# Kernel tuning notes

Measured on AMD Instinct MI355X. Metric: run time of the kernel, lower is better.

The kernel has to match this reference:

```python
import jax, jax.numpy as jnp
import numpy as np

N_NODES = 10000
N_EDGES = 320000
F_NODE = 16
NUM_BESSEL = 8
M = 32           # env_embed_multiplicity
LAT = 128        # latent dimension
R_MAX = 5.0
P_CUT = 6.0      # polynomial cutoff order
AVG_NEIGH = 32.0
SQRT3 = 1.7320508075688772
SQRT2 = 1.4142135623730951


def _mlp(x, weights):
    # nequip ScalarMLPFunction: linear layers with 1/sqrt(fan_in) norm, silu between layers
    h = x
    n = len(weights)
    for i, W in enumerate(weights):
        h = h @ W * (1.0 / np.sqrt(W.shape[0]))
        if i < n - 1:
            h = jax.nn.silu(h)
    return h


def _weight_channels(Y, w):
    # MakeWeightedChannels: Y [E,4] = (0e | 1e), w [E,M,2] per-irrep weights -> [E,M,4]
    return jnp.concatenate([w[..., 0:1] * Y[:, None, 0:1],
                            w[..., 1:2] * Y[:, None, 1:4]], axis=-1)


def setup_inputs():
    key = jax.random.key(0)
    ks = jax.random.split(key, 16)

    def w(k, i, o):
        return jax.random.normal(k, (i, o), jnp.float32)

    two_body_in = 2 * F_NODE + NUM_BESSEL  # 40
    return {
        "coordinates": jax.random.uniform(ks[0], (N_NODES, 3), jnp.float32),
        "node_attrs": jax.random.uniform(ks[1], (N_NODES, F_NODE), jnp.float32),
        "edge_index": jax.random.randint(ks[2], (2, N_EDGES), 0, N_NODES),
        "W2b0": w(ks[3], two_body_in, 64),
        "W2b1": w(ks[4], 64, 128),
        "W2b2": w(ks[5], 128, LAT),
        "Wenv0": w(ks[6], LAT, 4 * M),       # initial-edge embed + env weights (2 irreps each)
        "Wlat0": w(ks[7], LAT + 2 * M, 128),
        "Wlat1": w(ks[8], 128, LAT),
        "Ws0": w(ks[9], 2 * M, M),            # e3nn Linear, scalar block (2 paths)
        "Wv0": w(ks[10], 3 * M, M),           # e3nn Linear, vector block (3 paths)
        "Wenv1": w(ks[11], LAT, 2 * M),
        "Wfin0": w(ks[12], LAT + 2 * M, 128),
        "Wfin1": w(ks[13], 128, LAT),
    }


def reference(coordinates, node_attrs, edge_index, W2b0, W2b1, W2b2, Wenv0,
              Wlat0, Wlat1, Ws0, Wv0, Wenv1, Wfin0, Wfin1):
    sender, center = edge_index[0], edge_index[1]
    vec = coordinates[center] - coordinates[sender]            # [E,3]
    r = jnp.sqrt(jnp.sum(vec * vec, axis=-1) + 1e-12)          # [E]
    u = r / R_MAX
    p = P_CUT
    fcut = (1.0 - (p + 1.0) * (p + 2.0) / 2.0 * u**p
            + p * (p + 2.0) * u**(p + 1.0)
            - p * (p + 1.0) / 2.0 * u**(p + 2.0))
    fcut = jnp.where(u < 1.0, fcut, 0.0)
    n = jnp.arange(1, NUM_BESSEL + 1, dtype=jnp.float32)
    bessel = np.sqrt(2.0 / R_MAX) * jnp.sin(n * jnp.pi * u[:, None]) / r[:, None]
    edge_feats = bessel * fcut[:, None]                        # [E,8]
    unit = vec / r[:, None]
    Y = jnp.concatenate([jnp.ones_like(r)[:, None], SQRT3 * unit], axis=-1)  # [E,4] component-normalized SH

    inv_sqrt_n = 1.0 / np.sqrt(AVG_NEIGH)
    E = r.shape[0]

    # two-body latent (layer 0)
    lat_in = jnp.concatenate([node_attrs[center], node_attrs[sender], edge_feats], -1)
    lat = _mlp(lat_in, (W2b0, W2b1, W2b2)) * fcut[:, None]     # [E,LAT]
    w_all = lat @ Wenv0 * (1.0 / np.sqrt(LAT))                 # [E,4M]
    w_edge = w_all[:, :2 * M].reshape(E, M, 2)
    w_env = w_all[:, 2 * M:].reshape(E, M, 2)
    feat = _weight_channels(Y, w_edge)                         # [E,M,4] initial edge embed
    env = jax.ops.segment_sum(_weight_channels(Y, w_env), center, num_segments=N_NODES)
    env = env[center] * inv_sqrt_n                             # [E,M,4]

    fs, fv = feat[..., 0], feat[..., 1:]
    es, ev = env[..., 0], env[..., 1:]
    # layer-0 tensor product instruction list (uuu, no weights)
    p0 = fs * es                               # 0e x 0e -> 0e
    p1 = jnp.sum(fv * ev, -1) / SQRT3          # 1e x 1e -> 0e
    p2 = fs[..., None] * ev                    # 0e x 1e -> 1e
    p3 = fv * es[..., None]                    # 1e x 0e -> 1e
    p4 = jnp.cross(fv, ev) / SQRT2             # 1e x 1e -> 1e
    scal0 = jnp.concatenate([p0, p1], -1)      # [E,2M] scalar outs (n_scalar_outs=2)
    # per-layer e3nn Linear
    s_mix = scal0 @ Ws0 * (1.0 / np.sqrt(2 * M))                         # [E,M]
    v_mix = jnp.einsum('eic,io->eoc', jnp.concatenate([p2, p3, p4], 1), Wv0) * (1.0 / np.sqrt(3 * M))  # [E,M,3]

    # latent resnet update (update param 0 -> sigmoid = 0.5)
    alpha = 0.5
    c_old = 1.0 / np.sqrt(alpha * alpha + 1.0)
    c_new = alpha * c_old
    new_lat = _mlp(jnp.concatenate([lat, scal0], -1), (Wlat0, Wlat1)) * fcut[:, None]
    lat = c_old * lat + c_new * new_lat

    # layer 1 env embedding + tensor product (last layer -> scalars only)
    w_env1 = (lat @ Wenv1 * (1.0 / np.sqrt(LAT))).reshape(E, M, 2)
    env1 = jax.ops.segment_sum(_weight_channels(Y, w_env1), center, num_segments=N_NODES)
    env1 = env1[center] * inv_sqrt_n
    q0 = s_mix * env1[..., 0]
    q1 = jnp.sum(v_mix * env1[..., 1:], -1) / SQRT3
    scal1 = jnp.concatenate([q0, q1], -1)      # [E,2M]

    new_lat = _mlp(jnp.concatenate([lat, scal1], -1), (Wfin0, Wfin1)) * fcut[:, None]
    lat = c_old * lat + c_new * new_lat

    node_out = jax.ops.segment_sum(lat, center, num_segments=N_NODES) * inv_sqrt_n
    return node_out
```

## Files before the change

kernel.cpp:

```cpp
#include <hip/hip_runtime.h>
#include <hip/hip_bf16.h>
#include <math.h>

typedef __hip_bfloat16 bf16;
typedef __attribute__((ext_vector_type(8))) short short8;
typedef __attribute__((ext_vector_type(4))) float floatx4;

#define AMODE_PLAIN  0
#define AMODE_CONCAT 2
#define EPI_SPLIT    1
#define EPI_STORE    2
#define EPI_FCUT     3
#define EPI_RESID    4

#define INV_SQRT_N 0.17677669529663687f
#define INV_SQRT3  0.5773502691896258f
#define INV_SQRT2  0.7071067811865476f
#define C_OLD      0.8944271909999159f
#define C_NEW      0.4472135954999579f
#define PI_F       3.14159265358979323846f
#define SQRT3_F    1.7320508075688772f
#define BESSEL_PREF 0.6324555320336759f

__device__ __forceinline__ float b2f(bf16 x) { return __bfloat162float(x); }
__device__ __forceinline__ bf16  f2b(float x) { return __float2bfloat16(x); }
__device__ __forceinline__ unsigned short f2bu(float x) {
  bf16 h = f2b(x); unsigned short u; __builtin_memcpy(&u, &h, 2); return u;
}
__device__ __forceinline__ float silu_f(float v) { return v / (1.f + __expf(-v)); }
__device__ __forceinline__ floatx4 mfma16(short8 a, short8 b, floatx4 c) {
  return __builtin_amdgcn_mfma_f32_16x16x32_bf16(a, b, c, 0, 0, 0);
}

__global__ __launch_bounds__(256) void k_geom(
    const float* __restrict__ coords, const float* __restrict__ nattr,
    const int* __restrict__ eidx, int E,
    float* __restrict__ fcut, float* __restrict__ Yb, bf16* __restrict__ a40) {
  int e = blockIdx.x * 256 + threadIdx.x;
  if (e >= E) return;
  int s = eidx[e], c = eidx[E + e];
  float dx = coords[c*3+0] - coords[s*3+0];
  float dy = coords[c*3+1] - coords[s*3+1];
  float dz = coords[c*3+2] - coords[s*3+2];
  float r = sqrtf(dx*dx + dy*dy + dz*dz + 1e-12f);
  float u = r * 0.2f;
  float u3 = u*u*u;
  float u6 = u3*u3, u7 = u6*u, u8 = u7*u;
  float fc = 1.f - 28.f*u6 + 48.f*u7 - 21.f*u8;
  fc = (u < 1.f) ? fc : 0.f;
  float inv_r = 1.f / r;
  fcut[e] = fc;
  Yb[e*4+0] = 1.f;
  Yb[e*4+1] = SQRT3_F * dx * inv_r;
  Yb[e*4+2] = SQRT3_F * dy * inv_r;
  Yb[e*4+3] = SQRT3_F * dz * inv_r;
  bf16* row = a40 + (long)e * 40;
  #pragma unroll
  for (int i = 0; i < 16; ++i) row[i]      = f2b(nattr[(long)c*16 + i]);
  #pragma unroll
  for (int i = 0; i < 16; ++i) row[16 + i] = f2b(nattr[(long)s*16 + i]);
  float pref = BESSEL_PREF * inv_r * fc;
  #pragma unroll
  for (int n = 1; n <= 8; ++n)
    row[32 + n - 1] = f2b(pref * sinf((float)n * PI_F * u));
}

__global__ __launch_bounds__(256) void k_deg(
    const int* __restrict__ eidx, int E, int* __restrict__ deg) {
  int e = blockIdx.x * 256 + threadIdx.x;
  if (e < E) atomicAdd(&deg[eidx[E + e]], 1);
}

__global__ __launch_bounds__(1024) void k_scan(
    const int* __restrict__ deg, int N,
    int* __restrict__ rowptr, int* __restrict__ cursor) {
  __shared__ int part[1024];
  int t = threadIdx.x;
  int C = (N + 1023) / 1024;
  int base = t * C;
  int s = 0;
  for (int i = 0; i < C; ++i) { int idx = base + i; if (idx < N) s += deg[idx]; }
  part[t] = s;
  __syncthreads();
  for (int off = 1; off < 1024; off <<= 1) {
    int v = (t >= off) ? part[t - off] : 0;
    __syncthreads();
    part[t] += v;
    __syncthreads();
  }
  int excl = (t == 0) ? 0 : part[t - 1];
  for (int i = 0; i < C; ++i) {
    int idx = base + i;
    if (idx < N) { rowptr[idx] = excl; cursor[idx] = excl; excl += deg[idx]; }
  }
  if (t == 0) rowptr[N] = part[1023];
}

__global__ __launch_bounds__(256) void k_fill(
    const int* __restrict__ eidx, int E, int* __restrict__ cursor,
    int* __restrict__ eord) {
  int e = blockIdx.x * 256 + threadIdx.x;
  if (e >= E) return;
  int c = eidx[E + e];
  int slot = atomicAdd(&cursor[c], 1);
  eord[slot] = e;
}

__global__ __launch_bounds__(256) void k_wprep(
    const float* __restrict__ W, unsigned short* __restrict__ Wt, int K, int NOUT) {
  int t = blockIdx.x * 256 + threadIdx.x;
  if (t >= K * NOUT) return;
  int n = t / K, k = t % K;
  Wt[n * K + k] = f2bu(W[k * NOUT + n]);
}

__global__ __launch_bounds__(256) void k_wmix(
    const float* __restrict__ Ws0, const float* __restrict__ Wv0,
    unsigned short* __restrict__ Wm) {
  int t = blockIdx.x * 256 + threadIdx.x;
  if (t >= 32 * 160) return;
  int o = t / 160, k = t % 160;
  float v = (k < 64) ? Ws0[k * 32 + o] : Wv0[(k - 64) * 32 + o];
  Wm[o * 160 + k] = f2bu(v);
}

__global__ __launch_bounds__(256) void k_envg(
    const bf16* __restrict__ wenv, const float* __restrict__ Yb,
    const int* __restrict__ rowptr, const int* __restrict__ eord,
    int N, float* __restrict__ env) {
  int t = blockIdx.x * 256 + threadIdx.x;
  if (t >= N * 32) return;
  int n = t >> 5, m = t & 31;
  int j0 = rowptr[n], j1 = rowptr[n + 1];
  float a0 = 0.f, a1 = 0.f, a2 = 0.f, a3 = 0.f;
  for (int j = j0; j < j1; ++j) {
    int e = eord[j];
    float w0 = b2f(wenv[(long)e*64 + 2*m]);
    float w1 = b2f(wenv[(long)e*64 + 2*m + 1]);
    float4 y = *reinterpret_cast<const float4*>(&Yb[(long)e*4]);
    a0 += w0;
    a1 += w1 * y.y;
    a2 += w1 * y.z;
    a3 += w1 * y.w;
  }
  *reinterpret_cast<float4*>(&env[(long)n*128 + m*4]) = make_float4(a0, a1, a2, a3);
}

__global__ __launch_bounds__(256) void k_nodeg(
    const bf16* __restrict__ lat, const int* __restrict__ rowptr,
    const int* __restrict__ eord, int N, float* __restrict__ out) {
  int t = blockIdx.x * 256 + threadIdx.x;
  if (t >= N * 128) return;
  int n = t >> 7, j = t & 127;
  int j0 = rowptr[n], j1 = rowptr[n + 1];
  float s = 0.f;
  for (int q = j0; q < j1; ++q) {
    int e = eord[q];
    s += b2f(lat[(long)e*128 + j]);
  }
  out[t] = s * INV_SQRT_N;
}

__global__ __launch_bounds__(256) void mgemm40(
    const bf16* __restrict__ A, const unsigned short* __restrict__ Wt,
    bf16* __restrict__ out, float scale, int E) {
  __shared__ __align__(16) unsigned short As[64 * 72];
  __shared__ __align__(16) unsigned short Bs[64 * 72];
  int tid = threadIdx.x;
  int lane = tid & 63, w = tid >> 6;
  int nl = lane & 15, quad = lane >> 4;
  long e0 = (long)blockIdx.x * 64;

  for (int i = tid; i < 512; i += 256) {
    int e = i >> 3, h = i & 7;
    short8 v = {0,0,0,0,0,0,0,0};
    long eg = e0 + e;
    if (h < 5 && eg < E) v = *(const short8*)(A + eg * 40 + h * 8);
    *(short8*)&As[e * 72 + h * 8] = v;
  }
  for (int i = tid; i < 512; i += 256) {
    int n = i >> 3, h = i & 7;
    short8 v = {0,0,0,0,0,0,0,0};
    if (h < 5) v = *(const short8*)(Wt + n * 40 + h * 8);
    *(short8*)&Bs[n * 72 + h * 8] = v;
  }
  __syncthreads();

  floatx4 acc[4];
  #pragma unroll
  for (int i = 0; i < 4; ++i) acc[i] = (floatx4){0.f,0.f,0.f,0.f};
  #pragma unroll
  for (int ks = 0; ks < 2; ++ks) {
    short8 af[4];
    #pragma unroll
    for (int et = 0; et < 4; ++et)
      af[et] = *(const short8*)&As[(et*16 + nl) * 72 + ks*32 + quad*8];
    short8 bv = *(const short8*)&Bs[(w*16 + nl) * 72 + ks*32 + quad*8];
    #pragma unroll
    for (int et = 0; et < 4; ++et) acc[et] = mfma16(af[et], bv, acc[et]);
  }
  #pragma unroll
  for (int et = 0; et < 4; ++et)
    #pragma unroll
    for (int r = 0; r < 4; ++r) {
      long eg = e0 + et*16 + quad*4 + r;
      if (eg >= E) continue;
      out[eg * 64 + w*16 + nl] = f2b(silu_f(acc[et][r] * scale));
    }
}

template<int K, int NOUT, int EPI>
__global__ __launch_bounds__(256) void mgemm(
    const bf16* __restrict__ A, const unsigned short* __restrict__ Wt,
    bf16* __restrict__ out1, bf16* __restrict__ out2, float scale, int E) {
  constexpr int KP = 40;
  constexpr int CT = NOUT / 64;
  __shared__ __align__(16) unsigned short As[64 * KP];
  __shared__ __align__(16) unsigned short Bs[NOUT * KP];
  int tid = threadIdx.x;
  int lane = tid & 63, w = tid >> 6;
  int nl = lane & 15, quad = lane >> 4;
  long e0 = (long)blockIdx.x * 64;

  floatx4 acc[4][CT];
  #pragma unroll
  for (int i = 0; i < 4; ++i)
    #pragma unroll
    for (int j = 0; j < CT; ++j) acc[i][j] = (floatx4){0.f,0.f,0.f,0.f};

  int ae = tid & 63, akh = tid >> 6;
  long aeg = e0 + ae;

  for (int k0 = 0; k0 < K; k0 += 32) {
    if (k0) __syncthreads();
    {
      short8 v = {0,0,0,0,0,0,0,0};
      if (aeg < E) v = *(const short8*)(A + aeg * (long)K + k0 + akh * 8);
      *(short8*)&As[ae * KP + akh * 8] = v;
    }
    if constexpr (NOUT == 128) {
      int j = tid >> 1, h = tid & 1;
      const short8* s = (const short8*)(Wt + (long)j * K + k0 + h * 16);
      *(short8*)&Bs[j * KP + h * 16]     = s[0];
      *(short8*)&Bs[j * KP + h * 16 + 8] = s[1];
    } else {
      int j = tid >> 2, h = tid & 3;
      *(short8*)&Bs[j * KP + h * 8] =
          *(const short8*)(Wt + (long)j * K + k0 + h * 8);
    }
    __syncthreads();
    short8 af[4], bv[CT];
    #pragma unroll
    for (int et = 0; et < 4; ++et)
      af[et] = *(const short8*)&As[(et*16 + nl) * KP + quad * 8];
    #pragma unroll
    for (int ct = 0; ct < CT; ++ct)
      bv[ct] = *(const short8*)&Bs[(w*CT*16 + ct*16 + nl) * KP + quad * 8];
    #pragma unroll
    for (int et = 0; et < 4; ++et)
      #pragma unroll
      for (int ct = 0; ct < CT; ++ct)
        acc[et][ct] = mfma16(af[et], bv[ct], acc[et][ct]);
  }

  #pragma unroll
  for (int et = 0; et < 4; ++et)
    #pragma unroll
    for (int ct = 0; ct < CT; ++ct)
      #pragma unroll
      for (int r = 0; r < 4; ++r) {
        long eg = e0 + et*16 + quad*4 + r;
        if (eg >= E) continue;
        int col = w*CT*16 + ct*16 + nl;
        float v = acc[et][ct][r] * scale;
        if constexpr (EPI == EPI_SPLIT) {
          if (col < 64) out1[eg * 64 + col] = f2b(v);
          else          out2[eg * 64 + (col - 64)] = f2b(v);
        } else {
          out1[eg * NOUT + col] = f2b(v);
        }
      }
}

template<int K, int AMODE, int EPI>
__global__ __launch_bounds__(256) void mfused(
    const bf16* __restrict__ A, const bf16* __restrict__ A2,
    const unsigned short* __restrict__ W0t, const unsigned short* __restrict__ W1t,
    bf16* __restrict__ outb, const float* __restrict__ fcut,
    float scale0, float scale1, int E) {
  constexpr int KP = 40, HP = 136;
  __shared__ __align__(16) unsigned short As[64 * KP];
  __shared__ __align__(16) unsigned short Bs[128 * KP];
  __shared__ __align__(16) unsigned short Hs[64 * HP];
  int tid = threadIdx.x;
  int lane = tid & 63, w = tid >> 6;
  int nl = lane & 15, quad = lane >> 4;
  long e0 = (long)blockIdx.x * 64;

  floatx4 acc[4][2];
  #pragma unroll
  for (int i = 0; i < 4; ++i)
    #pragma unroll
    for (int j = 0; j < 2; ++j) acc[i][j] = (floatx4){0.f,0.f,0.f,0.f};

  int ae = tid & 63, akh = tid >> 6;
  long aeg = e0 + ae;
  int bj = tid >> 1, bh = tid & 1;

  for (int k0 = 0; k0 < K; k0 += 32) {
    if (k0) __syncthreads();
    {
      int kk = k0 + akh * 8;
      short8 v = {0,0,0,0,0,0,0,0};
      if (aeg < E) {
        const bf16* src;
        if constexpr (AMODE == AMODE_PLAIN) src = A + aeg * (long)K + kk;
        else src = (kk < 128) ? (A + aeg * 128 + kk) : (A2 + aeg * 64 + (kk - 128));
        v = *(const short8*)src;
      }
      *(short8*)&As[ae * KP + akh * 8] = v;
    }
    {
      const short8* s = (const short8*)(W0t + (long)bj * K + k0 + bh * 16);
      *(short8*)&Bs[bj * KP + bh * 16]     = s[0];
      *(short8*)&Bs[bj * KP + bh * 16 + 8] = s[1];
    }
    __syncthreads();
    short8 af[4], bv[2];
    #pragma unroll
    for (int et = 0; et < 4; ++et)
      af[et] = *(const short8*)&As[(et*16 + nl) * KP + quad * 8];
    #pragma unroll
    for (int ct = 0; ct < 2; ++ct)
      bv[ct] = *(const short8*)&Bs[(w*32 + ct*16 + nl) * KP + quad * 8];
    #pragma unroll
    for (int et = 0; et < 4; ++et)
      #pragma unroll
      for (int ct = 0; ct < 2; ++ct)
        acc[et][ct] = mfma16(af[et], bv[ct], acc[et][ct]);
  }

  #pragma unroll
  for (int et = 0; et < 4; ++et)
    #pragma unroll
    for (int ct = 0; ct < 2; ++ct)
      #pragma unroll
      for (int r = 0; r < 4; ++r) {
        int el = et*16 + quad*4 + r;
        int h  = w*32 + ct*16 + nl;
        Hs[el * HP + h] = f2bu(silu_f(acc[et][ct][r] * scale0));
      }
  #pragma unroll
  for (int i = 0; i < 4; ++i)
    #pragma unroll
    for (int j = 0; j < 2; ++j) acc[i][j] = (floatx4){0.f,0.f,0.f,0.f};

  for (int k0 = 0; k0 < 128; k0 += 32) {
    __syncthreads();
    {
      const short8* s = (const short8*)(W1t + (long)bj * 128 + k0 + bh * 16);
      *(short8*)&Bs[bj * KP + bh * 16]     = s[0];
      *(short8*)&Bs[bj * KP + bh * 16 + 8] = s[1];
    }
    __syncthreads();
    short8 af[4], bv[2];
    #pragma unroll
    for (int et = 0; et < 4; ++et)
      af[et] = *(const short8*)&Hs[(et*16 + nl) * HP + k0 + quad * 8];
    #pragma unroll
    for (int ct = 0; ct < 2; ++ct)
      bv[ct] = *(const short8*)&Bs[(w*32 + ct*16 + nl) * KP + quad * 8];
    #pragma unroll
    for (int et = 0; et < 4; ++et)
      #pragma unroll
      for (int ct = 0; ct < 2; ++ct)
        acc[et][ct] = mfma16(af[et], bv[ct], acc[et][ct]);
  }

  #pragma unroll
  for (int et = 0; et < 4; ++et)
    #pragma unroll
    for (int ct = 0; ct < 2; ++ct)
      #pragma unroll
      for (int r = 0; r < 4; ++r) {
        long eg = e0 + et*16 + quad*4 + r;
        if (eg >= E) continue;
        int col = w*32 + ct*16 + nl;
        float fc = fcut[eg];
        float v = acc[et][ct][r] * scale1 * fc;
        if constexpr (EPI == EPI_FCUT) {
          outb[eg * 128 + col] = f2b(v);
        } else {
          long idx = eg * 128 + col;
          outb[idx] = f2b(C_OLD * b2f(outb[idx]) + C_NEW * v);
        }
      }
}

__global__ __launch_bounds__(256) void k_prod(
    const bf16* __restrict__ wedge, const float* __restrict__ env,
    const float* __restrict__ Yb, const int* __restrict__ eidx, int E,
    bf16* __restrict__ scal) {
  long t = (long)blockIdx.x * 256 + threadIdx.x;
  if (t >= (long)E * 32) return;
  long e = t >> 5;
  int m = (int)(t & 31);
  int c = eidx[E + e];
  float w0 = b2f(wedge[e*64 + 2*m]), w1 = b2f(wedge[e*64 + 2*m + 1]);
  const float* ep = env + (long)c*128 + m*4;
  float es  = ep[0] * INV_SQRT_N;
  float evx = ep[1] * INV_SQRT_N, evy = ep[2] * INV_SQRT_N, evz = ep[3] * INV_SQRT_N;
  float y1 = Yb[e*4+1], y2 = Yb[e*4+2], y3 = Yb[e*4+3];
  float fvx = w1*y1, fvy = w1*y2, fvz = w1*y3;
  scal[e*64 + m]      = f2b(w0 * es);
  scal[e*64 + 32 + m] = f2b((fvx*evx + fvy*evy + fvz*evz) * INV_SQRT3);
}

__global__ __launch_bounds__(256) void k_mix2(
    const bf16* __restrict__ wedge, const float* __restrict__ env,
    const float* __restrict__ env1, const float* __restrict__ Yb,
    const int* __restrict__ eidx, const unsigned short* __restrict__ Wm,
    int E, bf16* __restrict__ scal) {
  constexpr int PP = 360;
  constexpr int RP = 132;
  __shared__ __align__(16) unsigned char SB[64 * PP * 2];
  __shared__ __align__(16) unsigned short Wl[32 * 160];
  unsigned short* P = (unsigned short*)SB;
  float* R = (float*)SB;
  int tid = threadIdx.x;
  int lane = tid & 63, w = tid >> 6;
  int nl = lane & 15, quad = lane >> 4;
  long e0 = (long)blockIdx.x * 64;

  for (int i = tid; i < 640; i += 256)
    *(short8*)&Wl[i * 8] = *(const short8*)(Wm + i * 8);

  int m = tid & 31;
  #pragma unroll
  for (int it = 0; it < 8; ++it) {
    int el = (tid >> 5) + it * 8;
    long e = e0 + el;
    if (e < E) {
      int c = eidx[E + e];
      float w0 = b2f(wedge[e*64 + 2*m]), w1 = b2f(wedge[e*64 + 2*m + 1]);
      float4 ev4 = *(const float4*)(env + (long)c*128 + m*4);
      float4 y   = *(const float4*)(Yb + e*4);
      float es  = ev4.x * INV_SQRT_N;
      float evx = ev4.y * INV_SQRT_N, evy = ev4.z * INV_SQRT_N, evz = ev4.w * INV_SQRT_N;
      float fvx = w1*y.y, fvy = w1*y.z, fvz = w1*y.w;
      unsigned short* p = P + el * PP;
      p[m]       = f2bu(w0 * es);
      p[32 + m]  = f2bu((fvx*evx + fvy*evy + fvz*evz) * INV_SQRT3);
      p[64 + m]  = f2bu(w0 * evx);
      p[96 + m]  = f2bu(fvx * es);
      p[128 + m] = f2bu((fvy*evz - fvz*evy) * INV_SQRT2);
      p[160 + m] = f2bu(w0 * evy);
      p[192 + m] = f2bu(fvy * es);
      p[224 + m] = f2bu((fvz*evx - fvx*evz) * INV_SQRT2);
      p[256 + m] = f2bu(w0 * evz);
      p[288 + m] = f2bu(fvz * es);
      p[320 + m] = f2bu((fvx*evy - fvy*evx) * INV_SQRT2);
    } else {
      unsigned short* p = P + el * PP;
      #pragma unroll
      for (int q = 0; q < 11; ++q) p[q*32 + m] = 0;
    }
  }
  __syncthreads();

  floatx4 acc[4][2];
  #pragma unroll
  for (int i = 0; i < 4; ++i)
    #pragma unroll
    for (int j = 0; j < 2; ++j) acc[i][j] = (floatx4){0.f,0.f,0.f,0.f};
  int pbase  = (w == 0) ? 0 : 64 + (w - 1) * 96;
  int wkbase = (w == 0) ? 0 : 64;
  int ksteps = (w == 0) ? 2 : 3;
  for (int ks = 0; ks < ksteps; ++ks) {
    short8 af[4], bv[2];
    #pragma unroll
    for (int et = 0; et < 4; ++et)
      af[et] = *(const short8*)&P[(et*16 + nl) * PP + pbase + ks*32 + quad*8];
    #pragma unroll
    for (int ct = 0; ct < 2; ++ct)
      bv[ct] = *(const short8*)&Wl[(ct*16 + nl) * 160 + wkbase + ks*32 + quad*8];
    #pragma unroll
    for (int et = 0; et < 4; ++et)
      #pragma unroll
      for (int ct = 0; ct < 2; ++ct)
        acc[et][ct] = mfma16(af[et], bv[ct], acc[et][ct]);
  }
  __syncthreads();

  #pragma unroll
  for (int et = 0; et < 4; ++et)
    #pragma unroll
    for (int ct = 0; ct < 2; ++ct)
      #pragma unroll
      for (int r = 0; r < 4; ++r) {
        int el = et*16 + quad*4 + r;
        R[el * RP + w*32 + ct*16 + nl] = acc[et][ct][r];
      }
  __syncthreads();

  #pragma unroll
  for (int it = 0; it < 8; ++it) {
    int el = (tid >> 5) + it * 8;
    long e = e0 + el;
    if (e >= E) continue;
    int o = m;
    int c = eidx[E + e];
    float4 e1 = *(const float4*)(env1 + (long)c*128 + o*4);
    float sr = R[el * RP + o];
    float vx = R[el * RP + 32 + o];
    float vy = R[el * RP + 64 + o];
    float vz = R[el * RP + 96 + o];
    float q0 = sr * 0.125f * (e1.x * INV_SQRT_N);
    float q1 = (vx*e1.y + vy*e1.z + vz*e1.w) *
               (0.10206207261596577f * INV_SQRT_N * INV_SQRT3);
    scal[e*64 + o]      = f2b(q0);
    scal[e*64 + 32 + o] = f2b(q1);
  }
}

extern "C" void kernel_launch(void* const* d_in, const int* in_sizes, int n_in,
                              void* d_out, int out_size, void* d_ws, size_t ws_size,
                              hipStream_t stream) {
  const float* coords = (const float*)d_in[0];
  const float* nattr  = (const float*)d_in[1];
  const int*   eidx   = (const int*)d_in[2];
  const float* W2b0   = (const float*)d_in[3];
  const float* W2b1   = (const float*)d_in[4];
  const float* W2b2   = (const float*)d_in[5];
  const float* Wenv0  = (const float*)d_in[6];
  const float* Wlat0  = (const float*)d_in[7];
  const float* Wlat1  = (const float*)d_in[8];
  const float* Ws0    = (const float*)d_in[9];
  const float* Wv0    = (const float*)d_in[10];
  const float* Wenv1  = (const float*)d_in[11];
  const float* Wfin0  = (const float*)d_in[12];
  const float* Wfin1  = (const float*)d_in[13];
  float* out = (float*)d_out;
  int E = in_sizes[2] / 2;
  int N = in_sizes[0] / 3;

  float* fcut   = (float*)d_ws;
  float* Yb     = fcut + (size_t)E;
  float* env    = Yb + (size_t)E*4;
  float* env1   = env + (size_t)N*128;
  int*   deg    = (int*)(env1 + (size_t)N*128);
  int*   rowptr = deg + N;
  int*   cursor = rowptr + (N + 8);
  int*   eord   = cursor + N;
  bf16*  b64    = (bf16*)(eord + E);
  bf16*  lat    = b64 + (size_t)E*64;
  bf16*  S      = lat + (size_t)E*128;
  unsigned short* W2b1t  = (unsigned short*)(S + (size_t)E*64);
  unsigned short* W2b2t  = W2b1t + 128*64;
  unsigned short* Wenv0t = W2b2t + 128*128;
  unsigned short* Wlat0t = Wenv0t + 128*128;
  unsigned short* Wlat1t = Wlat0t + 128*192;
  unsigned short* Wenv1t = Wlat1t + 128*128;
  unsigned short* Wfin0t = Wenv1t + 64*128;
  unsigned short* Wfin1t = Wfin0t + 128*192;
  unsigned short* W2b0t  = Wfin1t + 128*128;
  unsigned short* Wmixt  = W2b0t + 64*40;

  hipMemsetAsync(deg, 0, (size_t)N * sizeof(int), stream);

  dim3 blk(256);
  const float s40  = 0.15811388300841897f;
  const float s64  = 0.125f;
  const float s128 = 0.08838834764831845f;
  const float s192 = 0.07216878364870323f;
  int gB = (E + 63) / 64;
  int gE = (E + 255) / 256;

  k_geom<<<gE, blk, 0, stream>>>(coords, nattr, eidx, E, fcut, Yb, S );
  k_deg<<<gE, blk, 0, stream>>>(eidx, E, deg);
  k_scan<<<1, 1024, 0, stream>>>(deg, N, rowptr, cursor);
  k_fill<<<gE, blk, 0, stream>>>(eidx, E, cursor, eord);
  k_wprep<<<(64*128 + 255)/256,  blk, 0, stream>>>(W2b1,  W2b1t,  64, 128);
  k_wprep<<<(128*128 + 255)/256, blk, 0, stream>>>(W2b2,  W2b2t,  128, 128);
  k_wprep<<<(128*128 + 255)/256, blk, 0, stream>>>(Wenv0, Wenv0t, 128, 128);
  k_wprep<<<(192*128 + 255)/256, blk, 0, stream>>>(Wlat0, Wlat0t, 192, 128);
  k_wprep<<<(128*128 + 255)/256, blk, 0, stream>>>(Wlat1, Wlat1t, 128, 128);
  k_wprep<<<(128*64 + 255)/256,  blk, 0, stream>>>(Wenv1, Wenv1t, 128, 64);
  k_wprep<<<(192*128 + 255)/256, blk, 0, stream>>>(Wfin0, Wfin0t, 192, 128);
  k_wprep<<<(128*128 + 255)/256, blk, 0, stream>>>(Wfin1, Wfin1t, 128, 128);
  k_wprep<<<(40*64 + 255)/256,   blk, 0, stream>>>(W2b0,  W2b0t,  40, 64);
  k_wmix<<<(32*160 + 255)/256,   blk, 0, stream>>>(Ws0, Wv0, Wmixt);

  mgemm40<<<gB, blk, 0, stream>>>(S , W2b0t, b64, s40, E);
  mfused<64,AMODE_PLAIN,EPI_FCUT><<<gB, blk, 0, stream>>>(
      b64, nullptr, W2b1t, W2b2t, lat, fcut, s64, s128, E);

  mgemm<128,128,EPI_SPLIT><<<gB, blk, 0, stream>>>(
      lat, Wenv0t, b64, S , s128, E);

  k_envg<<<dim3((N*32 + 255) / 256), blk, 0, stream>>>(
      S , Yb, rowptr, eord, N, env);

  k_prod<<<dim3((int)(((long)E*32 + 255) / 256)), blk, 0, stream>>>(
      b64, env, Yb, eidx, E, S );

  mfused<192,AMODE_CONCAT,EPI_RESID><<<gB, blk, 0, stream>>>(
      lat, S , Wlat0t, Wlat1t, lat, fcut, s192, s128, E);

  mgemm<128,64,EPI_STORE><<<gB, blk, 0, stream>>>(
      lat, Wenv1t, S , nullptr, s128, E);

  k_envg<<<dim3((N*32 + 255) / 256), blk, 0, stream>>>(
      S , Yb, rowptr, eord, N, env1);

  k_mix2<<<gB, blk, 0, stream>>>(
      b64, env, env1, Yb, eidx, Wmixt, E, S );

  mfused<192,AMODE_CONCAT,EPI_RESID><<<gB, blk, 0, stream>>>(
      lat, S , Wfin0t, Wfin1t, lat, fcut, s192, s128, E);

  k_nodeg<<<dim3((N*128 + 255) / 256), blk, 0, stream>>>(
      lat, rowptr, eord, N, out);
}
```

Before: 829.1 us.

## Process edges in center-sorted order and merge weight prep kernels

The geometry kernel now writes every per-edge buffer in CSR (center-sorted) order, so all later edge kernels work on sorted edges. The gather-style segment reductions (env and node output) can then read contiguous rows instead of going through the eord indirection. A cent array replaces the eidx center lookups, which also gives the env gathers better locality. The ten weight-transpose launches are folded into one kernel to cut launch overhead. The sorted order is set by the atomic fill order, so it is not deterministic from run to run.

New measurement: 724.1 us. 12.7% less time.

```diff
diff --git a/kernel.cpp b/kernel.cpp
--- a/kernel.cpp
+++ b/kernel.cpp
@@ -30,39 +30,6 @@
 __device__ __forceinline__ float silu_f(float v) { return v / (1.f + __expf(-v)); }
 __device__ __forceinline__ floatx4 mfma16(short8 a, short8 b, floatx4 c) {
   return __builtin_amdgcn_mfma_f32_16x16x32_bf16(a, b, c, 0, 0, 0);
-}
-
-__global__ __launch_bounds__(256) void k_geom(
-    const float* __restrict__ coords, const float* __restrict__ nattr,
-    const int* __restrict__ eidx, int E,
-    float* __restrict__ fcut, float* __restrict__ Yb, bf16* __restrict__ a40) {
-  int e = blockIdx.x * 256 + threadIdx.x;
-  if (e >= E) return;
-  int s = eidx[e], c = eidx[E + e];
-  float dx = coords[c*3+0] - coords[s*3+0];
-  float dy = coords[c*3+1] - coords[s*3+1];
-  float dz = coords[c*3+2] - coords[s*3+2];
-  float r = sqrtf(dx*dx + dy*dy + dz*dz + 1e-12f);
-  float u = r * 0.2f;
-  float u3 = u*u*u;
-  float u6 = u3*u3, u7 = u6*u, u8 = u7*u;
-  float fc = 1.f - 28.f*u6 + 48.f*u7 - 21.f*u8;
-  fc = (u < 1.f) ? fc : 0.f;
-  float inv_r = 1.f / r;
-  fcut[e] = fc;
-  Yb[e*4+0] = 1.f;
-  Yb[e*4+1] = SQRT3_F * dx * inv_r;
-  Yb[e*4+2] = SQRT3_F * dy * inv_r;
-  Yb[e*4+3] = SQRT3_F * dz * inv_r;
-  bf16* row = a40 + (long)e * 40;
-  #pragma unroll
-  for (int i = 0; i < 16; ++i) row[i]      = f2b(nattr[(long)c*16 + i]);
-  #pragma unroll
-  for (int i = 0; i < 16; ++i) row[16 + i] = f2b(nattr[(long)s*16 + i]);
-  float pref = BESSEL_PREF * inv_r * fc;
-  #pragma unroll
-  for (int n = 1; n <= 8; ++n)
-    row[32 + n - 1] = f2b(pref * sinf((float)n * PI_F * u));
 }
 
 __global__ __launch_bounds__(256) void k_deg(
@@ -98,46 +65,93 @@
 
 __global__ __launch_bounds__(256) void k_fill(
     const int* __restrict__ eidx, int E, int* __restrict__ cursor,
-    int* __restrict__ eord) {
+    int* __restrict__ eord, int* __restrict__ cent) {
   int e = blockIdx.x * 256 + threadIdx.x;
   if (e >= E) return;
   int c = eidx[E + e];
   int slot = atomicAdd(&cursor[c], 1);
   eord[slot] = e;
-}
-
-__global__ __launch_bounds__(256) void k_wprep(
-    const float* __restrict__ W, unsigned short* __restrict__ Wt, int K, int NOUT) {
-  int t = blockIdx.x * 256 + threadIdx.x;
-  if (t >= K * NOUT) return;
+  cent[slot] = c;
+}
+
+__global__ __launch_bounds__(256) void k_geom(
+    const float* __restrict__ coords, const float* __restrict__ nattr,
+    const int* __restrict__ eidx, const int* __restrict__ eord, int E,
+    float* __restrict__ fcut, float* __restrict__ Yb, bf16* __restrict__ a40) {
+  int j = blockIdx.x * 256 + threadIdx.x;
+  if (j >= E) return;
+  int e = eord[j];
+  int s = eidx[e], c = eidx[E + e];
+  float dx = coords[c*3+0] - coords[s*3+0];
+  float dy = coords[c*3+1] - coords[s*3+1];
+  float dz = coords[c*3+2] - coords[s*3+2];
+  float r = sqrtf(dx*dx + dy*dy + dz*dz + 1e-12f);
+  float u = r * 0.2f;
+  float u3 = u*u*u;
+  float u6 = u3*u3, u7 = u6*u, u8 = u7*u;
+  float fc = 1.f - 28.f*u6 + 48.f*u7 - 21.f*u8;
+  fc = (u < 1.f) ? fc : 0.f;
+  float inv_r = 1.f / r;
+  fcut[j] = fc;
+  Yb[j*4+0] = 1.f;
+  Yb[j*4+1] = SQRT3_F * dx * inv_r;
+  Yb[j*4+2] = SQRT3_F * dy * inv_r;
+  Yb[j*4+3] = SQRT3_F * dz * inv_r;
+  bf16* row = a40 + (long)j * 40;
+  #pragma unroll
+  for (int i = 0; i < 16; ++i) row[i]      = f2b(nattr[(long)c*16 + i]);
+  #pragma unroll
+  for (int i = 0; i < 16; ++i) row[16 + i] = f2b(nattr[(long)s*16 + i]);
+  float pref = BESSEL_PREF * inv_r * fc;
+  #pragma unroll
+  for (int n = 1; n <= 8; ++n)
+    row[32 + n - 1] = f2b(pref * sinf((float)n * PI_F * u));
+}
+
+__device__ __forceinline__ void wp(const float* W, unsigned short* Wt,
+                                   int K, int NOUT, int t) {
   int n = t / K, k = t % K;
   Wt[n * K + k] = f2bu(W[k * NOUT + n]);
 }
 
-__global__ __launch_bounds__(256) void k_wmix(
-    const float* __restrict__ Ws0, const float* __restrict__ Wv0,
-    unsigned short* __restrict__ Wm) {
+__global__ __launch_bounds__(256) void k_wprep_all(
+    const float* W2b0, const float* W2b1, const float* W2b2,
+    const float* Wenv0, const float* Wlat0, const float* Wlat1,
+    const float* Wenv1, const float* Wfin0, const float* Wfin1,
+    const float* Ws0, const float* Wv0,
+    unsigned short* W2b0t, unsigned short* W2b1t, unsigned short* W2b2t,
+    unsigned short* Wenv0t, unsigned short* Wlat0t, unsigned short* Wlat1t,
+    unsigned short* Wenv1t, unsigned short* Wfin0t, unsigned short* Wfin1t,
+    unsigned short* Wmixt) {
   int t = blockIdx.x * 256 + threadIdx.x;
-  if (t >= 32 * 160) return;
-  int o = t / 160, k = t % 160;
-  float v = (k < 64) ? Ws0[k * 32 + o] : Wv0[(k - 64) * 32 + o];
-  Wm[o * 160 + k] = f2bu(v);
+  if (t < 8192)  { wp(W2b1,  W2b1t,  64, 128, t); return; } t -= 8192;
+  if (t < 16384) { wp(W2b2,  W2b2t, 128, 128, t); return; } t -= 16384;
+  if (t < 16384) { wp(Wenv0, Wenv0t,128, 128, t); return; } t -= 16384;
+  if (t < 24576) { wp(Wlat0, Wlat0t,192, 128, t); return; } t -= 24576;
+  if (t < 16384) { wp(Wlat1, Wlat1t,128, 128, t); return; } t -= 16384;
+  if (t < 8192)  { wp(Wenv1, Wenv1t,128,  64, t); return; } t -= 8192;
+  if (t < 24576) { wp(Wfin0, Wfin0t,192, 128, t); return; } t -= 24576;
+  if (t < 16384) { wp(Wfin1, Wfin1t,128, 128, t); return; } t -= 16384;
+  if (t < 2560)  { wp(W2b0,  W2b0t,  40,  64, t); return; } t -= 2560;
+  if (t < 5120) {
+    int o = t / 160, k = t % 160;
+    float v = (k < 64) ? Ws0[k * 32 + o] : Wv0[(k - 64) * 32 + o];
+    Wmixt[o * 160 + k] = f2bu(v);
+  }
 }
 
 __global__ __launch_bounds__(256) void k_envg(
     const bf16* __restrict__ wenv, const float* __restrict__ Yb,
-    const int* __restrict__ rowptr, const int* __restrict__ eord,
-    int N, float* __restrict__ env) {
+    const int* __restrict__ rowptr, int N, float* __restrict__ env) {
   int t = blockIdx.x * 256 + threadIdx.x;
   if (t >= N * 32) return;
   int n = t >> 5, m = t & 31;
   int j0 = rowptr[n], j1 = rowptr[n + 1];
   float a0 = 0.f, a1 = 0.f, a2 = 0.f, a3 = 0.f;
   for (int j = j0; j < j1; ++j) {
-    int e = eord[j];
-    float w0 = b2f(wenv[(long)e*64 + 2*m]);
-    float w1 = b2f(wenv[(long)e*64 + 2*m + 1]);
-    float4 y = *reinterpret_cast<const float4*>(&Yb[(long)e*4]);
+    float w0 = b2f(wenv[(long)j*64 + 2*m]);
+    float w1 = b2f(wenv[(long)j*64 + 2*m + 1]);
+    float4 y = *reinterpret_cast<const float4*>(&Yb[(long)j*4]);
     a0 += w0;
     a1 += w1 * y.y;
     a2 += w1 * y.z;
@@ -148,16 +162,14 @@
 
 __global__ __launch_bounds__(256) void k_nodeg(
     const bf16* __restrict__ lat, const int* __restrict__ rowptr,
-    const int* __restrict__ eord, int N, float* __restrict__ out) {
+    int N, float* __restrict__ out) {
   int t = blockIdx.x * 256 + threadIdx.x;
   if (t >= N * 128) return;
   int n = t >> 7, j = t & 127;
   int j0 = rowptr[n], j1 = rowptr[n + 1];
   float s = 0.f;
-  for (int q = j0; q < j1; ++q) {
-    int e = eord[q];
-    s += b2f(lat[(long)e*128 + j]);
-  }
+  for (int q = j0; q < j1; ++q)
+    s += b2f(lat[(long)q*128 + j]);
   out[t] = s * INV_SQRT_N;
 }
 
@@ -399,13 +411,13 @@
 
 __global__ __launch_bounds__(256) void k_prod(
     const bf16* __restrict__ wedge, const float* __restrict__ env,
-    const float* __restrict__ Yb, const int* __restrict__ eidx, int E,
+    const float* __restrict__ Yb, const int* __restrict__ cent, int E,
     bf16* __restrict__ scal) {
   long t = (long)blockIdx.x * 256 + threadIdx.x;
   if (t >= (long)E * 32) return;
   long e = t >> 5;
   int m = (int)(t & 31);
-  int c = eidx[E + e];
+  int c = cent[e];
   float w0 = b2f(wedge[e*64 + 2*m]), w1 = b2f(wedge[e*64 + 2*m + 1]);
   const float* ep = env + (long)c*128 + m*4;
   float es  = ep[0] * INV_SQRT_N;
@@ -419,7 +431,7 @@
 __global__ __launch_bounds__(256) void k_mix2(
     const bf16* __restrict__ wedge, const float* __restrict__ env,
     const float* __restrict__ env1, const float* __restrict__ Yb,
-    const int* __restrict__ eidx, const unsigned short* __restrict__ Wm,
+    const int* __restrict__ cent, const unsigned short* __restrict__ Wm,
     int E, bf16* __restrict__ scal) {
   constexpr int PP = 360;
   constexpr int RP = 132;
@@ -441,7 +453,7 @@
     int el = (tid >> 5) + it * 8;
     long e = e0 + el;
     if (e < E) {
-      int c = eidx[E + e];
+      int c = cent[e];
       float w0 = b2f(wedge[e*64 + 2*m]), w1 = b2f(wedge[e*64 + 2*m + 1]);
       float4 ev4 = *(const float4*)(env + (long)c*128 + m*4);
       float4 y   = *(const float4*)(Yb + e*4);
@@ -509,7 +521,7 @@
     long e = e0 + el;
     if (e >= E) continue;
     int o = m;
-    int c = eidx[E + e];
+    int c = cent[e];
     float4 e1 = *(const float4*)(env1 + (long)c*128 + o*4);
     float sr = R[el * RP + o];
     float vx = R[el * RP + 32 + o];
@@ -552,7 +564,8 @@
   int*   rowptr = deg + N;
   int*   cursor = rowptr + (N + 8);
   int*   eord   = cursor + N;
-  bf16*  b64    = (bf16*)(eord + E);
+  int*   cent   = eord + E;
+  bf16*  b64    = (bf16*)(cent + E);
   bf16*  lat    = b64 + (size_t)E*64;
   bf16*  S      = lat + (size_t)E*128;
   unsigned short* W2b1t  = (unsigned short*)(S + (size_t)E*64);
@@ -576,20 +589,13 @@
   int gB = (E + 63) / 64;
   int gE = (E + 255) / 256;
 
-  k_geom<<<gE, blk, 0, stream>>>(coords, nattr, eidx, E, fcut, Yb, S );
   k_deg<<<gE, blk, 0, stream>>>(eidx, E, deg);
   k_scan<<<1, 1024, 0, stream>>>(deg, N, rowptr, cursor);
-  k_fill<<<gE, blk, 0, stream>>>(eidx, E, cursor, eord);
-  k_wprep<<<(64*128 + 255)/256,  blk, 0, stream>>>(W2b1,  W2b1t,  64, 128);
-  k_wprep<<<(128*128 + 255)/256, blk, 0, stream>>>(W2b2,  W2b2t,  128, 128);
-  k_wprep<<<(128*128 + 255)/256, blk, 0, stream>>>(Wenv0, Wenv0t, 128, 128);
-  k_wprep<<<(192*128 + 255)/256, blk, 0, stream>>>(Wlat0, Wlat0t, 192, 128);
-  k_wprep<<<(128*128 + 255)/256, blk, 0, stream>>>(Wlat1, Wlat1t, 128, 128);
-  k_wprep<<<(128*64 + 255)/256,  blk, 0, stream>>>(Wenv1, Wenv1t, 128, 64);
-  k_wprep<<<(192*128 + 255)/256, blk, 0, stream>>>(Wfin0, Wfin0t, 192, 128);
-  k_wprep<<<(128*128 + 255)/256, blk, 0, stream>>>(Wfin1, Wfin1t, 128, 128);
-  k_wprep<<<(40*64 + 255)/256,   blk, 0, stream>>>(W2b0,  W2b0t,  40, 64);
-  k_wmix<<<(32*160 + 255)/256,   blk, 0, stream>>>(Ws0, Wv0, Wmixt);
+  k_fill<<<gE, blk, 0, stream>>>(eidx, E, cursor, eord, cent);
+  k_geom<<<gE, blk, 0, stream>>>(coords, nattr, eidx, eord, E, fcut, Yb, S );
+  k_wprep_all<<<dim3(542), blk, 0, stream>>>(
+      W2b0, W2b1, W2b2, Wenv0, Wlat0, Wlat1, Wenv1, Wfin0, Wfin1, Ws0, Wv0,
+      W2b0t, W2b1t, W2b2t, Wenv0t, Wlat0t, Wlat1t, Wenv1t, Wfin0t, Wfin1t, Wmixt);
 
   mgemm40<<<gB, blk, 0, stream>>>(S , W2b0t, b64, s40, E);
   mfused<64,AMODE_PLAIN,EPI_FCUT><<<gB, blk, 0, stream>>>(
@@ -599,10 +605,10 @@
       lat, Wenv0t, b64, S , s128, E);
 
   k_envg<<<dim3((N*32 + 255) / 256), blk, 0, stream>>>(
-      S , Yb, rowptr, eord, N, env);
+      S , Yb, rowptr, N, env);
 
   k_prod<<<dim3((int)(((long)E*32 + 255) / 256)), blk, 0, stream>>>(
-      b64, env, Yb, eidx, E, S );
+      b64, env, Yb, cent, E, S );
 
   mfused<192,AMODE_CONCAT,EPI_RESID><<<gB, blk, 0, stream>>>(
       lat, S , Wlat0t, Wlat1t, lat, fcut, s192, s128, E);
@@ -611,14 +617,14 @@
       lat, Wenv1t, S , nullptr, s128, E);
 
   k_envg<<<dim3((N*32 + 255) / 256), blk, 0, stream>>>(
-      S , Yb, rowptr, eord, N, env1);
+      S , Yb, rowptr, N, env1);
 
   k_mix2<<<gB, blk, 0, stream>>>(
-      b64, env, env1, Yb, eidx, Wmixt, E, S );
+      b64, env, env1, Yb, cent, Wmixt, E, S );
 
   mfused<192,AMODE_CONCAT,EPI_RESID><<<gB, blk, 0, stream>>>(
       lat, S , Wfin0t, Wfin1t, lat, fcut, s192, s128, E);
 
   k_nodeg<<<dim3((N*128 + 255) / 256), blk, 0, stream>>>(
-      lat, rowptr, eord, N, out);
-}
+      lat, rowptr, N, out);
+}
```
